# Kernel tuning notes

Hardware: AMD Instinct MI355X
Metric: run time of the kernel (lower is better)

## Reference

```python
import jax, jax.numpy as jnp
import numpy as np

N_NODES = 100000
N_EDGES = 1600000
IN_CH, GCN_CH, OUT_CH = 64, 64, 32


def gcn_conv(x, W, b, row, col, ew):
    """PyG GCNConv: normalize=True, add_self_loops=True (weight 1.0)."""
    N = x.shape[0]
    deg = jax.ops.segment_sum(ew, col, num_segments=N) + 1.0  # self-loop weight 1
    dis = jax.lax.rsqrt(deg)                                   # deg >= 1
    norm = dis[row] * ew * dis[col]                            # [E]
    xw = x @ W                                                 # [N, C_out]
    agg = jax.ops.segment_sum(norm[:, None] * xw[row], col, num_segments=N)
    # self-loop contribution: dis[i] * 1 * dis[i] * xw[i]
    return agg + (dis * dis)[:, None] * xw + b


def setup_inputs() -> dict:
    key = jax.random.key(0)
    ks = jax.random.split(key, 9)
    x = jax.random.normal(ks[0], (N_NODES, IN_CH), dtype=jnp.float32)
    edge_index = jax.random.randint(ks[1], (2, N_EDGES), 0, N_NODES, dtype=jnp.int64)
    edge_weight = jax.random.uniform(ks[2], (N_EDGES,), dtype=jnp.float32)
    s1 = 1.0 / np.sqrt(IN_CH)
    s2 = 1.0 / np.sqrt(GCN_CH)
    W1 = jax.random.uniform(ks[3], (IN_CH, GCN_CH), jnp.float32, -s1, s1)
    b1 = jnp.zeros((GCN_CH,), jnp.float32)
    W2 = jax.random.uniform(ks[4], (GCN_CH, GCN_CH), jnp.float32, -s2, s2)
    b2 = jnp.zeros((GCN_CH,), jnp.float32)
    Wout = jax.random.uniform(ks[5], (GCN_CH, OUT_CH), jnp.float32, -s2, s2)
    bout = jax.random.uniform(ks[6], (OUT_CH,), jnp.float32, -s2, s2)
    return {"x": x, "edge_index": edge_index, "edge_weight": edge_weight,
            "W1": W1, "b1": b1, "W2": W2, "b2": b2, "Wout": Wout, "bout": bout}


def reference(x, edge_index, edge_weight, W1, b1, W2, b2, Wout, bout):
    row, col = edge_index[0], edge_index[1]
    h = jax.nn.relu(gcn_conv(x, W1, b1, row, col, edge_weight))
    h = jax.nn.relu(gcn_conv(h, W2, b2, row, col, edge_weight))
    return jnp.tanh(h @ Wout + bout)
```

## Files before the change

### kernel.cpp

```cpp
#include <hip/hip_runtime.h>
#include <hip/hip_fp16.h>
#include <math.h>

#define N_NODES 100000
#define N_EDGES 1600000
#define IN_CH   64
#define GCN_CH  64
#define OUT_CH  32
#define MAXDEG  48

#define EW_SCALE  32768.0f
#define EW_INV    (1.0f / 32768.0f)

#define BSHIFT   7
#define NBUCK    1024
#define NBUCK_USED ((N_NODES + 127) / 128)
#define EPB      4096
#define NBLK     ((N_EDGES + EPB - 1) / EPB)
#define HIST_TOT (NBUCK * NBLK)
#define NCHUNK   (HIST_TOT / 1024)

typedef _Float16 f16x2 __attribute__((ext_vector_type(2)));

__device__ inline float fdot2(__half2 a, __half2 b, float c) {
    f16x2 av, bv;
    __builtin_memcpy(&av, &a, 4);
    __builtin_memcpy(&bv, &b, 4);
    return __builtin_amdgcn_fdot2(av, bv, c, false);
}

__global__ void hist_kernel(const int* __restrict__ col, unsigned* __restrict__ hist_g) {
    __shared__ unsigned sh[NBUCK];
    int blk = blockIdx.x;
    for (int i = threadIdx.x; i < NBUCK; i += 1024) sh[i] = 0;
    __syncthreads();
    int base = blk * EPB;
    int lim  = min(EPB, N_EDGES - base);
    for (int i = threadIdx.x; i < lim; i += 1024)
        atomicAdd(&sh[(unsigned)col[base + i] >> BSHIFT], 1u);
    __syncthreads();
    for (int b = threadIdx.x; b < NBUCK; b += 1024)
        hist_g[(size_t)b * NBLK + blk] = sh[b];
}

__global__ void scan1_kernel(const unsigned* __restrict__ in, unsigned* __restrict__ outp,
                             unsigned* __restrict__ blockSums) {
    __shared__ unsigned sdata[256];
    int t = threadIdx.x;
    int base = blockIdx.x * 1024 + t * 4;
    unsigned v[4];
    unsigned sum = 0;
#pragma unroll
    for (int i = 0; i < 4; ++i) { v[i] = in[base + i]; sum += v[i]; }
    sdata[t] = sum;
    __syncthreads();
    for (int off = 1; off < 256; off <<= 1) {
        unsigned x = (t >= off) ? sdata[t - off] : 0;
        __syncthreads();
        sdata[t] += x;
        __syncthreads();
    }
    unsigned excl = sdata[t] - sum;
    if (t == 255) blockSums[blockIdx.x] = sdata[t];
    unsigned run = excl;
#pragma unroll
    for (int i = 0; i < 4; ++i) { outp[base + i] = run; run += v[i]; }
}

__global__ void scan2_kernel(unsigned* __restrict__ blockSums) {
    __shared__ unsigned s[512];
    int t = threadIdx.x;
    unsigned orig = (t < NCHUNK) ? blockSums[t] : 0;
    s[t] = orig;
    __syncthreads();
    for (int off = 1; off < 512; off <<= 1) {
        unsigned x = (t >= off) ? s[t - off] : 0;
        __syncthreads();
        s[t] += x;
        __syncthreads();
    }
    if (t < NCHUNK) blockSums[t] = s[t] - orig;
}

__global__ void scatter_kernel(const int* __restrict__ row, const int* __restrict__ col,
                               const float* __restrict__ ew,
                               const unsigned* __restrict__ scanned,
                               const unsigned* __restrict__ blockSums,
                               unsigned long long* __restrict__ srt) {
    __shared__ unsigned cur[NBUCK];
    int blk = blockIdx.x;
    for (int b = threadIdx.x; b < NBUCK; b += 1024) {
        size_t hidx = (size_t)b * NBLK + blk;
        cur[b] = scanned[hidx] + blockSums[hidx >> 10];
    }
    __syncthreads();
    int base = blk * EPB;
    int lim  = min(EPB, N_EDGES - base);
    for (int i = threadIdx.x; i < lim; i += 1024) {
        int e = base + i;
        unsigned c = (unsigned)col[e];
        unsigned r = (unsigned)row[e];
        float    w = ew[e];
        unsigned u15 = min((unsigned)(w * EW_SCALE + 0.5f), 32767u);
        unsigned rec = (r << 15) | u15;
        unsigned pos = atomicAdd(&cur[c >> BSHIFT], 1u);
        srt[pos] = ((unsigned long long)c << 32) | rec;
    }
}

__global__ void ell_fill_kernel(const unsigned* __restrict__ scanned,
                                const unsigned* __restrict__ blockSums,
                                const unsigned long long* __restrict__ srt,
                                unsigned* __restrict__ ell,
                                unsigned* __restrict__ deg_arr, float* __restrict__ dis) {
    __shared__ unsigned cur[128];
    __shared__ float    wsum[128];
    int b = blockIdx.x;
    if (threadIdx.x < 128) { cur[threadIdx.x] = 0; wsum[threadIdx.x] = 0.f; }
    __syncthreads();
    size_t h0 = (size_t)b * NBLK;
    size_t h1 = (size_t)(b + 1) * NBLK;
    unsigned start = scanned[h0] + blockSums[h0 >> 10];
    unsigned end   = (b + 1 < NBUCK) ? (scanned[h1] + blockSums[h1 >> 10])
                                     : (unsigned)N_EDGES;
    for (unsigned i = start + threadIdx.x; i < end; i += 256) {
        unsigned long long v = srt[i];
        unsigned c   = (unsigned)(v >> 32);
        unsigned rec = (unsigned)v;
        unsigned cl  = c & 127u;
        unsigned k   = atomicAdd(&cur[cl], 1u);
        if (k < MAXDEG) ell[(size_t)c * MAXDEG + k] = rec;
        atomicAdd(&wsum[cl], (float)(rec & 32767u) * EW_INV);
    }
    __syncthreads();
    if (threadIdx.x < 128) {
        int c = b * 128 + threadIdx.x;
        if (c < N_NODES) {
            deg_arr[c] = min(cur[threadIdx.x], (unsigned)MAXDEG);
            dis[c]     = rsqrtf(wsum[threadIdx.x] + 1.0f);
        }
    }
}

__global__ void gemm64_f16_kernel(const float* __restrict__ X, const float* __restrict__ W,
                                  __half* __restrict__ Y, int nrows) {
    __shared__ float4 Ws[64][16];
    int t = threadIdx.x;
    for (int i = t; i < 64 * 16; i += 256)
        ((float4*)Ws)[i] = ((const float4*)W)[i];
    __syncthreads();

    int q   = t & 15;
    int sub = t >> 4;
    int row = blockIdx.x * 16 + sub;
    if (row >= nrows) return;
    const float4* xr = (const float4*)(X + (size_t)row * 64);
    float4 acc = {0.f, 0.f, 0.f, 0.f};
#pragma unroll
    for (int k4 = 0; k4 < 16; ++k4) {
        float4 xv = xr[k4];
#pragma unroll
        for (int j = 0; j < 4; ++j) {
            float xs = (j == 0) ? xv.x : (j == 1) ? xv.y : (j == 2) ? xv.z : xv.w;
            float4 wv = Ws[k4 * 4 + j][q];
            acc.x = fmaf(xs, wv.x, acc.x);
            acc.y = fmaf(xs, wv.y, acc.y);
            acc.z = fmaf(xs, wv.z, acc.z);
            acc.w = fmaf(xs, wv.w, acc.w);
        }
    }
    union { __half2 h[2]; float2 f; } u;
    u.h[0] = __floats2half2_rn(acc.x, acc.y);
    u.h[1] = __floats2half2_rn(acc.z, acc.w);
    *(float2*)(Y + (size_t)row * 64 + q * 4) = u.f;
}

__global__ void gemm64h_f16_kernel(const __half* __restrict__ X, const float* __restrict__ W,
                                   __half* __restrict__ Y, int nrows) {
    __shared__ float4 Ws[64][16];
    int t = threadIdx.x;
    for (int i = t; i < 64 * 16; i += 256)
        ((float4*)Ws)[i] = ((const float4*)W)[i];
    __syncthreads();

    int q   = t & 15;
    int sub = t >> 4;
    int row = blockIdx.x * 16 + sub;
    if (row >= nrows) return;
    const float4* xr = (const float4*)(X + (size_t)row * 64);
    float4 acc = {0.f, 0.f, 0.f, 0.f};
#pragma unroll
    for (int k8 = 0; k8 < 8; ++k8) {
        float4 raw = xr[k8];
        const __half2* hp = (const __half2*)&raw;
#pragma unroll
        for (int j = 0; j < 4; ++j) {
            float xs0 = __low2float(hp[j]);
            float xs1 = __high2float(hp[j]);
            float4 w0 = Ws[k8 * 8 + 2 * j][q];
            float4 w1 = Ws[k8 * 8 + 2 * j + 1][q];
            acc.x = fmaf(xs0, w0.x, acc.x); acc.y = fmaf(xs0, w0.y, acc.y);
            acc.z = fmaf(xs0, w0.z, acc.z); acc.w = fmaf(xs0, w0.w, acc.w);
            acc.x = fmaf(xs1, w1.x, acc.x); acc.y = fmaf(xs1, w1.y, acc.y);
            acc.z = fmaf(xs1, w1.z, acc.z); acc.w = fmaf(xs1, w1.w, acc.w);
        }
    }
    union { __half2 h[2]; float2 f; } u;
    u.h[0] = __floats2half2_rn(acc.x, acc.y);
    u.h[1] = __floats2half2_rn(acc.z, acc.w);
    *(float2*)(Y + (size_t)row * 64 + q * 4) = u.f;
}

__device__ inline void make_h_raw(const float* acc, float4 xraw,
                                  const float* b, int q, float dd, float* h) {
    const __half2* hp = (const __half2*)&xraw;
    float4 b0 = *(const float4*)(b + q * 8);
    float4 b1 = *(const float4*)(b + q * 8 + 4);
    float xs[8] = {__low2float(hp[0]), __high2float(hp[0]),
                   __low2float(hp[1]), __high2float(hp[1]),
                   __low2float(hp[2]), __high2float(hp[2]),
                   __low2float(hp[3]), __high2float(hp[3])};
    float bb[8] = {b0.x, b0.y, b0.z, b0.w, b1.x, b1.y, b1.z, b1.w};
#pragma unroll
    for (int i = 0; i < 8; ++i)
        h[i] = fmaxf(fmaf(dd, xs[i], acc[i]) + bb[i], 0.f);
}

__device__ inline void fma_pk(float4 raw, __half2 nv, __half2* acc) {
    const __half2* ha = (const __half2*)&raw;
    acc[0] = __hfma2(nv, ha[0], acc[0]);
    acc[1] = __hfma2(nv, ha[1], acc[1]);
    acc[2] = __hfma2(nv, ha[2], acc[2]);
    acc[3] = __hfma2(nv, ha[3], acc[3]);
}

__device__ inline void gather_core(int node, int lane,
                                   const unsigned* __restrict__ deg_arr,
                                   const unsigned* __restrict__ ell,
                                   const __half* __restrict__ XWh,
                                   const float* __restrict__ dis,
                                   float& dc_out, float4& xself, float* accf) {
    int half = lane >> 5;
    int l    = lane & 31;
    int g    = l >> 3;
    int q    = l & 7;
    int base = half << 5;

    int deg = (int)deg_arr[node];
    const unsigned* erow = ell + (size_t)node * MAXDEG;
    unsigned rec1 = (l < deg) ? erow[l] : 0u;
    unsigned rec2 = (l < 16 && 32 + l < deg) ? erow[32 + l] : 0u;
    float dc = dis[node];
    dc_out = dc;

    int   src1 = (int)(rec1 >> 15);
    float nv1  = dis[src1] * ((float)(rec1 & 32767u) * EW_INV) * dc;
    int   src2 = (int)(rec2 >> 15);
    float nv2  = dis[src2] * ((float)(rec2 & 32767u) * EW_INV) * dc;
    __half2 t1 = __float2half2_rn(nv1), t2 = __float2half2_rn(nv2);
    int nv1pk, nv2pk;
    __builtin_memcpy(&nv1pk, &t1, 4);
    __builtin_memcpy(&nv2pk, &t2, 4);

    xself = *(const float4*)(XWh + (size_t)node * 64 + q * 8);

    int dmax = max(deg, __shfl_xor(deg, 32, 64));

    __half2 acc[4] = {__float2half2_rn(0.f), __float2half2_rn(0.f),
                      __float2half2_rn(0.f), __float2half2_rn(0.f)};
    int s1 = min(dmax, 32);
    for (int s = 0; s < s1; s += 8) {
        int srcA  = __shfl(src1,  base + s + g, 64);
        int nvA_i = __shfl(nv1pk, base + s + g, 64);
        int srcB  = __shfl(src1,  base + s + 4 + g, 64);
        int nvB_i = __shfl(nv1pk, base + s + 4 + g, 64);
        float4 rawA = *(const float4*)(XWh + (size_t)srcA * 64 + q * 8);
        float4 rawB = *(const float4*)(XWh + (size_t)srcB * 64 + q * 8);
        __half2 nvA, nvB;
        __builtin_memcpy(&nvA, &nvA_i, 4);
        __builtin_memcpy(&nvB, &nvB_i, 4);
        fma_pk(rawA, nvA, acc);
        fma_pk(rawB, nvB, acc);
    }
    if (dmax > 32) {
        for (int s = 32; s < dmax; s += 4) {
            int srcB  = __shfl(src2,  base + (s - 32) + g, 64);
            int nvB_i = __shfl(nv2pk, base + (s - 32) + g, 64);
            float4 raw = *(const float4*)(XWh + (size_t)srcB * 64 + q * 8);
            __half2 nvB; __builtin_memcpy(&nvB, &nvB_i, 4);
            fma_pk(raw, nvB, acc);
        }
    }
#pragma unroll
    for (int m = 8; m <= 16; m <<= 1) {
#pragma unroll
        for (int i = 0; i < 4; ++i) {
            int ai; __builtin_memcpy(&ai, &acc[i], 4);
            int bi = __shfl_xor(ai, m, 64);
            __half2 bh; __builtin_memcpy(&bh, &bi, 4);
            acc[i] = __hadd2(acc[i], bh);
        }
    }
#pragma unroll
    for (int i = 0; i < 4; ++i) {
        accf[2 * i]     = __low2float(acc[i]);
        accf[2 * i + 1] = __high2float(acc[i]);
    }
}

__global__ void gather_h_kernel(const unsigned* __restrict__ deg_arr,
                                const unsigned* __restrict__ ell,
                                const __half* __restrict__ XWh,
                                const float* __restrict__ dis, const float* __restrict__ b,
                                __half* __restrict__ H) {
    int lane = threadIdx.x & 63;
    int node = blockIdx.x * 16 + (threadIdx.x >> 6) * 2 + (lane >> 5);
    int l = lane & 31;
    int q = l & 7;

    float dc; float4 xself; float accf[8];
    gather_core(node, lane, deg_arr, ell, XWh, dis, dc, xself, accf);

    if ((l >> 3) == 0) {
        float h[8];
        make_h_raw(accf, xself, b, q, dc * dc, h);
        union { __half2 hh[4]; float4 f; } u;
        u.hh[0] = __floats2half2_rn(h[0], h[1]);
        u.hh[1] = __floats2half2_rn(h[2], h[3]);
        u.hh[2] = __floats2half2_rn(h[4], h[5]);
        u.hh[3] = __floats2half2_rn(h[6], h[7]);
        *(float4*)(H + (size_t)node * 64 + q * 8) = u.f;
    }
}

__global__ void gather_out_kernel(const unsigned* __restrict__ deg_arr,
                                  const unsigned* __restrict__ ell,
                                  const __half* __restrict__ XWh,
                                  const float* __restrict__ dis, const float* __restrict__ b,
                                  const float* __restrict__ Wout, const float* __restrict__ bout,
                                  float* __restrict__ OUT) {
    __shared__ __half2 Ws2[32][32];
    {
        for (int idx = threadIdx.x; idx < 32 * 32; idx += (int)blockDim.x) {
            int kp = idx >> 5, j = idx & 31;
            Ws2[kp][j] = __floats2half2_rn(Wout[(2 * kp) * OUT_CH + j],
                                           Wout[(2 * kp + 1) * OUT_CH + j]);
        }
        __syncthreads();
    }

    int lane = threadIdx.x & 63;
    int node = blockIdx.x * 16 + (threadIdx.x >> 6) * 2 + (lane >> 5);
    int half = lane >> 5;
    int l = lane & 31;
    int q = l & 7;
    int base = half << 5;

    float dc; float4 xself; float accf[8];
    gather_core(node, lane, deg_arr, ell, XWh, dis, dc, xself, accf);

    float h[8];
    make_h_raw(accf, xself, b, q, dc * dc, h);

    int hpk[4];
#pragma unroll
    for (int i = 0; i < 4; ++i) {
        __half2 t2 = __floats2half2_rn(h[2 * i], h[2 * i + 1]);
        __builtin_memcpy(&hpk[i], &t2, 4);
    }
    float partial = 0.f;
#pragma unroll
    for (int kk = 0; kk < 32; ++kk) {
        int hv_i = __shfl(hpk[kk & 3], base + (kk >> 2), 64);
        __half2 hv; __builtin_memcpy(&hv, &hv_i, 4);
        partial = fdot2(hv, Ws2[kk][l], partial);
    }
    float v = partial + bout[l];
    float e = __expf(2.f * v);
    OUT[(size_t)node * OUT_CH + l] = 1.f - 2.f / (e + 1.f);
}

extern "C" void kernel_launch(void* const* d_in, const int* in_sizes, int n_in,
                              void* d_out, int out_size, void* d_ws, size_t ws_size,
                              hipStream_t stream) {
    const float* x     = (const float*)d_in[0];
    const int*   eidx  = (const int*)  d_in[1];
    const float* ew    = (const float*)d_in[2];
    const float* W1    = (const float*)d_in[3];
    const float* b1    = (const float*)d_in[4];
    const float* W2    = (const float*)d_in[5];
    const float* b2    = (const float*)d_in[6];
    const float* Wout  = (const float*)d_in[7];
    const float* bout  = (const float*)d_in[8];
    float*       out   = (float*)d_out;

    const int* row = eidx;
    const int* col = eidx + N_EDGES;

    char*  ws   = (char*)d_ws;
    size_t offs = 0;
    auto alloc = [&](size_t bytes) {
        char* p = ws + offs;
        offs += (bytes + 1023) & ~(size_t)1023;
        return p;
    };
    unsigned* hist_g    = (unsigned*)alloc((size_t)HIST_TOT * sizeof(unsigned));
    unsigned* scanned   = (unsigned*)alloc((size_t)HIST_TOT * sizeof(unsigned));
    unsigned* blockSums = (unsigned*)alloc((size_t)NCHUNK * sizeof(unsigned));
    unsigned long long* srt = (unsigned long long*)alloc((size_t)N_EDGES * 8);
    unsigned* deg_arr   = (unsigned*)alloc((size_t)N_NODES * sizeof(unsigned));
    float*    dis       = (float*)   alloc((size_t)N_NODES * sizeof(float));
    unsigned* ell       = (unsigned*)alloc((size_t)N_NODES * MAXDEG * sizeof(unsigned));
    __half*   xwh       = (__half*)  alloc((size_t)N_NODES * GCN_CH * sizeof(__half));
    __half*   hbuf      = (__half*)srt;

    const int BLK  = 256;
    const int BLKG = 512;
    const int gGemm   = (N_NODES + 15) / 16;
    const int gGather = N_NODES / 16;

    hist_kernel<<<NBLK, 1024, 0, stream>>>(col, hist_g);
    scan1_kernel<<<NCHUNK, 256, 0, stream>>>(hist_g, scanned, blockSums);
    scan2_kernel<<<1, 512, 0, stream>>>(blockSums);
    scatter_kernel<<<NBLK, 1024, 0, stream>>>(row, col, ew, scanned, blockSums, srt);
    ell_fill_kernel<<<NBUCK_USED, 256, 0, stream>>>(scanned, blockSums, srt,
                                                    ell, deg_arr, dis);

    gemm64_f16_kernel<<<gGemm, BLK, 0, stream>>>(x, W1, xwh, N_NODES);
    gather_h_kernel<<<gGather, BLKG, 0, stream>>>(deg_arr, ell, xwh, dis, b1, hbuf);

    gemm64h_f16_kernel<<<gGemm, BLK, 0, stream>>>(hbuf, W2, xwh, N_NODES);
    gather_out_kernel<<<gGather, BLKG, 0, stream>>>(deg_arr, ell, xwh, dis, b2,
                                                    Wout, bout, out);
}
```

Baseline: 164.4 us.

## Fuse chunk scan into scatter/ell_fill and co-schedule first GEMM with scatter

Removes the separate single-block scan2 kernel by having each scatter and ell_fill block redo the 512-entry chunk prefix scan in shared memory. The first-layer X@W1 GEMM is merged into the scatter launch as extra blocks, so it overlaps with the edge scatter and two launches disappear. ell_fill now runs 512 threads per block, and the gather's first-32-neighbour loop is unrolled to four loads per iteration. In exchange, every block repeats the redundant scan work with nine barriers, and gather blocks with fewer than 16 neighbours do wasted shuffles and loads.

Result: faster. 156.2 us (-5.0%).

```diff
diff --git a/kernel.cpp b/kernel.cpp
--- a/kernel.cpp
+++ b/kernel.cpp
@@ -19,6 +19,7 @@
 #define NBLK     ((N_EDGES + EPB - 1) / EPB)
 #define HIST_TOT (NBUCK * NBLK)
 #define NCHUNK   (HIST_TOT / 1024)
+#define GEMMB    ((N_NODES + 63) / 64)
 
 typedef _Float16 f16x2 __attribute__((ext_vector_type(2)));
 
@@ -67,44 +68,80 @@
     for (int i = 0; i < 4; ++i) { outp[base + i] = run; run += v[i]; }
 }
 
-__global__ void scan2_kernel(unsigned* __restrict__ blockSums) {
-    __shared__ unsigned s[512];
+__device__ inline void chunk_scan(const unsigned* __restrict__ bsum, unsigned* cb,
+                                  int t) {
+    if (t < 512) cb[t] = (t < NCHUNK) ? bsum[t] : 0u;
+    __syncthreads();
+    for (int off = 1; off < 512; off <<= 1) {
+        unsigned x = 0;
+        if (t < 512 && t >= off) x = cb[t - off];
+        __syncthreads();
+        if (t < 512) cb[t] += x;
+        __syncthreads();
+    }
+}
+
+__global__ void scatter_gemm_kernel(const int* __restrict__ row, const int* __restrict__ col,
+                                    const float* __restrict__ ew,
+                                    const unsigned* __restrict__ scanned,
+                                    const unsigned* __restrict__ blockSums,
+                                    unsigned long long* __restrict__ srt,
+                                    const float* __restrict__ X, const float* __restrict__ W,
+                                    __half* __restrict__ Y) {
+    __shared__ unsigned cur[NBUCK];
+    __shared__ unsigned cb[512];
+    __shared__ float4   Ws[64][16];
     int t = threadIdx.x;
-    unsigned orig = (t < NCHUNK) ? blockSums[t] : 0;
-    s[t] = orig;
-    __syncthreads();
-    for (int off = 1; off < 512; off <<= 1) {
-        unsigned x = (t >= off) ? s[t - off] : 0;
-        __syncthreads();
-        s[t] += x;
-        __syncthreads();
-    }
-    if (t < NCHUNK) blockSums[t] = s[t] - orig;
-}
-
-__global__ void scatter_kernel(const int* __restrict__ row, const int* __restrict__ col,
-                               const float* __restrict__ ew,
-                               const unsigned* __restrict__ scanned,
-                               const unsigned* __restrict__ blockSums,
-                               unsigned long long* __restrict__ srt) {
-    __shared__ unsigned cur[NBUCK];
-    int blk = blockIdx.x;
-    for (int b = threadIdx.x; b < NBUCK; b += 1024) {
-        size_t hidx = (size_t)b * NBLK + blk;
-        cur[b] = scanned[hidx] + blockSums[hidx >> 10];
-    }
-    __syncthreads();
-    int base = blk * EPB;
-    int lim  = min(EPB, N_EDGES - base);
-    for (int i = threadIdx.x; i < lim; i += 1024) {
-        int e = base + i;
-        unsigned c = (unsigned)col[e];
-        unsigned r = (unsigned)row[e];
-        float    w = ew[e];
-        unsigned u15 = min((unsigned)(w * EW_SCALE + 0.5f), 32767u);
-        unsigned rec = (r << 15) | u15;
-        unsigned pos = atomicAdd(&cur[c >> BSHIFT], 1u);
-        srt[pos] = ((unsigned long long)c << 32) | rec;
+    int bid = blockIdx.x;
+
+    if (bid < NBLK) {
+        chunk_scan(blockSums, cb, t);
+        int blk = bid;
+        for (int b = t; b < NBUCK; b += 1024) {
+            size_t hidx = (size_t)b * NBLK + blk;
+            unsigned chunk = (unsigned)(hidx >> 10);
+            cur[b] = scanned[hidx] + (chunk ? cb[chunk - 1] : 0u);
+        }
+        __syncthreads();
+        int base = blk * EPB;
+        int lim  = min(EPB, N_EDGES - base);
+        for (int i = t; i < lim; i += 1024) {
+            int e = base + i;
+            unsigned c = (unsigned)col[e];
+            unsigned r = (unsigned)row[e];
+            float    w = ew[e];
+            unsigned u15 = min((unsigned)(w * EW_SCALE + 0.5f), 32767u);
+            unsigned rec = (r << 15) | u15;
+            unsigned pos = atomicAdd(&cur[c >> BSHIFT], 1u);
+            srt[pos] = ((unsigned long long)c << 32) | rec;
+        }
+    } else {
+        ((float4*)Ws)[t] = ((const float4*)W)[t];
+        __syncthreads();
+        int gb  = bid - NBLK;
+        int q   = t & 15;
+        int sub = t >> 4;
+        int rw  = gb * 64 + sub;
+        if (rw >= N_NODES) return;
+        const float4* xr = (const float4*)(X + (size_t)rw * 64);
+        float4 acc = {0.f, 0.f, 0.f, 0.f};
+#pragma unroll
+        for (int k4 = 0; k4 < 16; ++k4) {
+            float4 xv = xr[k4];
+#pragma unroll
+            for (int j = 0; j < 4; ++j) {
+                float xs = (j == 0) ? xv.x : (j == 1) ? xv.y : (j == 2) ? xv.z : xv.w;
+                float4 wv = Ws[k4 * 4 + j][q];
+                acc.x = fmaf(xs, wv.x, acc.x);
+                acc.y = fmaf(xs, wv.y, acc.y);
+                acc.z = fmaf(xs, wv.z, acc.z);
+                acc.w = fmaf(xs, wv.w, acc.w);
+            }
+        }
+        union { __half2 h[2]; float2 f; } u;
+        u.h[0] = __floats2half2_rn(acc.x, acc.y);
+        u.h[1] = __floats2half2_rn(acc.z, acc.w);
+        *(float2*)(Y + (size_t)rw * 64 + q * 4) = u.f;
     }
 }
 
@@ -113,17 +150,21 @@
                                 const unsigned long long* __restrict__ srt,
                                 unsigned* __restrict__ ell,
                                 unsigned* __restrict__ deg_arr, float* __restrict__ dis) {
+    __shared__ unsigned cb[512];
     __shared__ unsigned cur[128];
     __shared__ float    wsum[128];
+    int t = threadIdx.x;
+    chunk_scan(blockSums, cb, t);
+    if (t < 128) { cur[t] = 0; wsum[t] = 0.f; }
+    __syncthreads();
     int b = blockIdx.x;
-    if (threadIdx.x < 128) { cur[threadIdx.x] = 0; wsum[threadIdx.x] = 0.f; }
-    __syncthreads();
     size_t h0 = (size_t)b * NBLK;
     size_t h1 = (size_t)(b + 1) * NBLK;
-    unsigned start = scanned[h0] + blockSums[h0 >> 10];
-    unsigned end   = (b + 1 < NBUCK) ? (scanned[h1] + blockSums[h1 >> 10])
+    unsigned c0 = (unsigned)(h0 >> 10), c1 = (unsigned)(h1 >> 10);
+    unsigned start = scanned[h0] + (c0 ? cb[c0 - 1] : 0u);
+    unsigned end   = (b + 1 < NBUCK) ? (scanned[h1] + (c1 ? cb[c1 - 1] : 0u))
                                      : (unsigned)N_EDGES;
-    for (unsigned i = start + threadIdx.x; i < end; i += 256) {
+    for (unsigned i = start + t; i < end; i += 512) {
         unsigned long long v = srt[i];
         unsigned c   = (unsigned)(v >> 32);
         unsigned rec = (unsigned)v;
@@ -133,46 +174,13 @@
         atomicAdd(&wsum[cl], (float)(rec & 32767u) * EW_INV);
     }
     __syncthreads();
-    if (threadIdx.x < 128) {
-        int c = b * 128 + threadIdx.x;
+    if (t < 128) {
+        int c = b * 128 + t;
         if (c < N_NODES) {
-            deg_arr[c] = min(cur[threadIdx.x], (unsigned)MAXDEG);
-            dis[c]     = rsqrtf(wsum[threadIdx.x] + 1.0f);
-        }
-    }
-}
-
-__global__ void gemm64_f16_kernel(const float* __restrict__ X, const float* __restrict__ W,
-                                  __half* __restrict__ Y, int nrows) {
-    __shared__ float4 Ws[64][16];
-    int t = threadIdx.x;
-    for (int i = t; i < 64 * 16; i += 256)
-        ((float4*)Ws)[i] = ((const float4*)W)[i];
-    __syncthreads();
-
-    int q   = t & 15;
-    int sub = t >> 4;
-    int row = blockIdx.x * 16 + sub;
-    if (row >= nrows) return;
-    const float4* xr = (const float4*)(X + (size_t)row * 64);
-    float4 acc = {0.f, 0.f, 0.f, 0.f};
-#pragma unroll
-    for (int k4 = 0; k4 < 16; ++k4) {
-        float4 xv = xr[k4];
-#pragma unroll
-        for (int j = 0; j < 4; ++j) {
-            float xs = (j == 0) ? xv.x : (j == 1) ? xv.y : (j == 2) ? xv.z : xv.w;
-            float4 wv = Ws[k4 * 4 + j][q];
-            acc.x = fmaf(xs, wv.x, acc.x);
-            acc.y = fmaf(xs, wv.y, acc.y);
-            acc.z = fmaf(xs, wv.z, acc.z);
-            acc.w = fmaf(xs, wv.w, acc.w);
-        }
-    }
-    union { __half2 h[2]; float2 f; } u;
-    u.h[0] = __floats2half2_rn(acc.x, acc.y);
-    u.h[1] = __floats2half2_rn(acc.z, acc.w);
-    *(float2*)(Y + (size_t)row * 64 + q * 4) = u.f;
+            deg_arr[c] = min(cur[t], (unsigned)MAXDEG);
+            dis[c]     = rsqrtf(wsum[t] + 1.0f);
+        }
+    }
 }
 
 __global__ void gemm64h_f16_kernel(const __half* __restrict__ X, const float* __restrict__ W,
@@ -269,18 +277,28 @@
     __half2 acc[4] = {__float2half2_rn(0.f), __float2half2_rn(0.f),
                       __float2half2_rn(0.f), __float2half2_rn(0.f)};
     int s1 = min(dmax, 32);
-    for (int s = 0; s < s1; s += 8) {
+    for (int s = 0; s < s1; s += 16) {
         int srcA  = __shfl(src1,  base + s + g, 64);
         int nvA_i = __shfl(nv1pk, base + s + g, 64);
         int srcB  = __shfl(src1,  base + s + 4 + g, 64);
         int nvB_i = __shfl(nv1pk, base + s + 4 + g, 64);
+        int srcC  = __shfl(src1,  base + s + 8 + g, 64);
+        int nvC_i = __shfl(nv1pk, base + s + 8 + g, 64);
+        int srcD  = __shfl(src1,  base + s + 12 + g, 64);
+        int nvD_i = __shfl(nv1pk, base + s + 12 + g, 64);
         float4 rawA = *(const float4*)(XWh + (size_t)srcA * 64 + q * 8);
         float4 rawB = *(const float4*)(XWh + (size_t)srcB * 64 + q * 8);
-        __half2 nvA, nvB;
+        float4 rawC = *(const float4*)(XWh + (size_t)srcC * 64 + q * 8);
+        float4 rawD = *(const float4*)(XWh + (size_t)srcD * 64 + q * 8);
+        __half2 nvA, nvB, nvC, nvD;
         __builtin_memcpy(&nvA, &nvA_i, 4);
         __builtin_memcpy(&nvB, &nvB_i, 4);
+        __builtin_memcpy(&nvC, &nvC_i, 4);
+        __builtin_memcpy(&nvD, &nvD_i, 4);
         fma_pk(rawA, nvA, acc);
         fma_pk(rawB, nvB, acc);
+        fma_pk(rawC, nvC, acc);
+        fma_pk(rawD, nvD, acc);
     }
     if (dmax > 32) {
         for (int s = 32; s < dmax; s += 4) {
@@ -421,12 +439,11 @@
 
     hist_kernel<<<NBLK, 1024, 0, stream>>>(col, hist_g);
     scan1_kernel<<<NCHUNK, 256, 0, stream>>>(hist_g, scanned, blockSums);
-    scan2_kernel<<<1, 512, 0, stream>>>(blockSums);
-    scatter_kernel<<<NBLK, 1024, 0, stream>>>(row, col, ew, scanned, blockSums, srt);
-    ell_fill_kernel<<<NBUCK_USED, 256, 0, stream>>>(scanned, blockSums, srt,
+    scatter_gemm_kernel<<<NBLK + GEMMB, 1024, 0, stream>>>(row, col, ew, scanned,
+                                                           blockSums, srt, x, W1, xwh);
+    ell_fill_kernel<<<NBUCK_USED, 512, 0, stream>>>(scanned, blockSums, srt,
                                                     ell, deg_arr, dis);
 
-    gemm64_f16_kernel<<<gGemm, BLK, 0, stream>>>(x, W1, xwh, N_NODES);
     gather_h_kernel<<<gGather, BLKG, 0, stream>>>(deg_arr, ell, xwh, dis, b1, hbuf);
 
     gemm64h_f16_kernel<<<gGemm, BLK, 0, stream>>>(hbuf, W2, xwh, N_NODES);
```
